# Kernel optimization log

Measured on AMD Instinct MI355X. Metric: run time of the kernel, lower is better.

Reference implementation:

```python
import jax, jax.numpy as jnp
import numpy as np

V = 50000   # vocab_size
D = 128     # embed_dim
B = 2048    # number of (center, contexts) pairs
C = 20      # context window size


def setup_inputs() -> dict:
    key = jax.random.key(0)
    ks = jax.random.split(key, 12)
    s = 0.05
    inp = {
        "center_id": jax.random.randint(ks[0], (B,), 0, V),
        "context_ids": jax.random.randint(ks[1], (B, C), 0, V),
        "epsilon": jax.random.normal(ks[2], (D,), dtype=jnp.float32),
        # parameters (torch Linear convention: W is [out, in])
        "embeddings": jax.random.normal(ks[3], (V, D), dtype=jnp.float32) * s,
        "prior_locs": jax.random.normal(ks[4], (V, D), dtype=jnp.float32) * s,
        "prior_scales": jax.random.normal(ks[5], (V, D), dtype=jnp.float32) * s,
        "W_enc": jax.random.normal(ks[6], (2 * D, 2 * D), dtype=jnp.float32) * s,
        "b_enc": jnp.zeros((2 * D,), dtype=jnp.float32),
        "W_loc": jax.random.normal(ks[7], (D, 2 * D), dtype=jnp.float32) * s,
        "b_loc": jnp.zeros((D,), dtype=jnp.float32),
        "W_scale": jax.random.normal(ks[8], (D, 2 * D), dtype=jnp.float32) * s,
        "b_scale": jnp.zeros((D,), dtype=jnp.float32),
        "W_vocab": jax.random.normal(ks[9], (V, D), dtype=jnp.float32) * s,
        "b_vocab": jnp.zeros((V,), dtype=jnp.float32),
    }
    return inp


def reference(center_id, context_ids, epsilon, embeddings, prior_locs, prior_scales,
              W_enc, b_enc, W_loc, b_loc, W_scale, b_scale, W_vocab, b_vocab):
    # Embedding lookups
    center_embed = embeddings[center_id]              # [B, D]
    context_embeds = embeddings[context_ids]          # [B, C, D]
    center_rep = jnp.broadcast_to(center_embed[:, None, :], context_embeds.shape)
    enc_in = jnp.concatenate([center_rep, context_embeds], axis=2)  # [B, C, 2D]

    # Encoder + sum over context
    h = jax.nn.relu(jnp.einsum('bcd,ed->bce', enc_in, W_enc) + b_enc)
    h = jnp.sum(h, axis=1)                            # [B, 2D]

    loc = h @ W_loc.T + b_loc                         # [B, D]
    scale = jax.nn.softplus(h @ W_scale.T + b_scale)  # [B, D]

    # Reparameterized sample (single shared epsilon, as in original)
    z = loc + scale * epsilon                         # [B, D]

    # Categorical over vocab; log-softmax == log(softmax) stably
    logits = z @ W_vocab.T + b_vocab                  # [B, V]
    log_cat = jax.nn.log_softmax(logits, axis=1)

    # Log-likelihood: sum_k log p(context_k | z)  (vectorized gather-reduce)
    lls = jnp.take_along_axis(log_cat, context_ids, axis=1).sum(axis=1)  # [B]

    # Closed-form diagonal-Gaussian KL( N(loc, scale^2) || N(ploc, pscale^2) )
    prior_loc = prior_locs[center_id]
    prior_scale = jax.nn.softplus(prior_scales[center_id])
    var0 = scale ** 2
    var1 = prior_scale ** 2
    kl = jnp.sum(jnp.log(prior_scale / scale) + (var0 + (loc - prior_loc) ** 2) / (2.0 * var1) - 0.5,
                 axis=1)                              # [B]

    elbo = lls - kl
    return jnp.mean(-elbo)
```

## Files before the change

kernel.cpp:

```cpp
#include <hip/hip_runtime.h>
#include <math.h>

#define VSZ 50000
#define VPAD 50176
#define DD  128
#define BB  2048
#define CC  20
#define E2  256

#define NCHK 98
#define CH_COLS 512
#define NRB 16
#define NWG (NCHK * NRB)

typedef short short8 __attribute__((ext_vector_type(8)));
typedef float f32x4  __attribute__((ext_vector_type(4)));

#define LOG2E 1.44269504f

__device__ __forceinline__ float softplusf(float x) {
  if (x > 20.f) return x;
  if (x < -20.f) return __expf(x);
  return log1pf(__expf(x));
}

__device__ __forceinline__ unsigned short f2bf(float f) {
  unsigned u = __float_as_uint(f);
  u = (u + 0x7fffu + ((u >> 16) & 1u)) >> 16;
  return (unsigned short)u;
}

__device__ __forceinline__ void gload_lds16(const void* g, void* l) {
  __builtin_amdgcn_global_load_lds(
      (const __attribute__((address_space(1))) unsigned int*)g,
      (__attribute__((address_space(3))) unsigned int*)l, 16, 0, 0);
}

#define NV4 1600000
#define NE4 16384
#define NL4 8192
__global__ __launch_bounds__(256) void convert_all_kernel(
    const float* __restrict__ Wv, const float* __restrict__ We,
    const float* __restrict__ Wl, const float* __restrict__ Wsc,
    ushort4* __restrict__ wv_bf, ushort4* __restrict__ we_bf,
    ushort4* __restrict__ wls_bf, float* __restrict__ S)
{
  const int gtid = blockIdx.x * 256 + threadIdx.x;
  const int stride = gridDim.x * 256;
  if (gtid < BB) S[gtid] = 0.f;
  if (gtid < (VPAD - VSZ) * 32) {
    ushort4 z; z.x = 0; z.y = 0; z.z = 0; z.w = 0;
    wv_bf[(size_t)VSZ * 32 + gtid] = z;
  }
  const int total = NV4 + NE4 + 2 * NL4;
  for (int idx = gtid; idx < total; idx += stride) {
    const float4* src; ushort4* dst; int off;
    if (idx < NV4)                   { src = (const float4*)Wv;  dst = wv_bf;  off = idx; }
    else if (idx < NV4 + NE4)        { src = (const float4*)We;  dst = we_bf;  off = idx - NV4; }
    else if (idx < NV4 + NE4 + NL4)  { src = (const float4*)Wl;  dst = wls_bf; off = idx - NV4 - NE4; }
    else { src = (const float4*)Wsc; dst = wls_bf + NL4;         off = idx - NV4 - NE4 - NL4; }
    float4 v = src[off];
    ushort4 o;
    o.x = f2bf(v.x); o.y = f2bf(v.y); o.z = f2bf(v.z); o.w = f2bf(v.w);
    dst[off] = o;
  }
}

__global__ __launch_bounds__(256) void enc_mfma_kernel(
    const int* __restrict__ center_id, const int* __restrict__ context_ids,
    const float* __restrict__ embeddings,
    const unsigned short* __restrict__ we_bf, const float* __restrict__ b_enc,
    unsigned short* __restrict__ h_bf)
{
  const int b    = blockIdx.x;
  const int tid  = threadIdx.x;
  const int wave = tid >> 6, lane = tid & 63;
  const int lr = lane & 15;
  const int lk = lane >> 4;

  __shared__ __align__(16) unsigned short ebd[21][136];

  for (int i = tid; i < 21 * 32; i += 256) {
    const int row = i >> 5, q = i & 31;
    const int src = (row < CC) ? context_ids[b * CC + row] : center_id[b];
    float4 v = ((const float4*)(embeddings + (size_t)src * DD))[q];
    ushort4 o;
    o.x = f2bf(v.x); o.y = f2bf(v.y); o.z = f2bf(v.z); o.w = f2bf(v.w);
    *(ushort4*)&ebd[row][q * 4] = o;
  }
  __syncthreads();

  f32x4 acc[2][4];
  #pragma unroll
  for (int rt = 0; rt < 2; rt++)
    #pragma unroll
    for (int ct = 0; ct < 4; ct++) acc[rt][ct] = (f32x4){0.f, 0.f, 0.f, 0.f};

  const bool r1ok = (16 + lr) < CC;

  #pragma unroll
  for (int step = 0; step < 4; step++) {
    const int k0 = step * 32 + lk * 8;
    short8 a = *(const short8*)&ebd[20][k0];
    #pragma unroll
    for (int ct = 0; ct < 4; ct++) {
      const int e = (wave * 4 + ct) * 16 + lr;
      short8 w = *(const short8*)(we_bf + (size_t)e * E2 + k0);
      acc[0][ct] = __builtin_amdgcn_mfma_f32_16x16x32_bf16(a, w, acc[0][ct], 0, 0, 0);
      acc[1][ct] = __builtin_amdgcn_mfma_f32_16x16x32_bf16(a, w, acc[1][ct], 0, 0, 0);
    }
  }
  #pragma unroll
  for (int step = 4; step < 8; step++) {
    const int k0 = step * 32 + lk * 8;
    const int kk = k0 - DD;
    short8 a0 = *(const short8*)&ebd[lr][kk];
    short8 a1 = r1ok ? *(const short8*)&ebd[16 + lr][kk] : (short8)0;
    #pragma unroll
    for (int ct = 0; ct < 4; ct++) {
      const int e = (wave * 4 + ct) * 16 + lr;
      short8 w = *(const short8*)(we_bf + (size_t)e * E2 + k0);
      acc[0][ct] = __builtin_amdgcn_mfma_f32_16x16x32_bf16(a0, w, acc[0][ct], 0, 0, 0);
      acc[1][ct] = __builtin_amdgcn_mfma_f32_16x16x32_bf16(a1, w, acc[1][ct], 0, 0, 0);
    }
  }

  float be[4], p[4];
  #pragma unroll
  for (int ct = 0; ct < 4; ct++) { be[ct] = b_enc[(wave * 4 + ct) * 16 + lr]; p[ct] = 0.f; }
  #pragma unroll
  for (int rt = 0; rt < 2; rt++) {
    #pragma unroll
    for (int j = 0; j < 4; j++) {
      const int row = rt * 16 + lk * 4 + j;
      if (row < CC) {
        #pragma unroll
        for (int ct = 0; ct < 4; ct++) p[ct] += fmaxf(acc[rt][ct][j] + be[ct], 0.f);
      }
    }
  }
  #pragma unroll
  for (int ct = 0; ct < 4; ct++) {
    p[ct] += __shfl_xor(p[ct], 16);
    p[ct] += __shfl_xor(p[ct], 32);
  }
  if (lk == 0) {
    #pragma unroll
    for (int ct = 0; ct < 4; ct++)
      h_bf[(size_t)b * E2 + (wave * 4 + ct) * 16 + lr] = f2bf(p[ct]);
  }
}

__global__ __launch_bounds__(256) void ls_post_kernel(
    const int* __restrict__ center_id, const int* __restrict__ context_ids,
    const float* __restrict__ eps,
    const float* __restrict__ prior_locs, const float* __restrict__ prior_scales,
    const unsigned short* __restrict__ h_bf, const unsigned short* __restrict__ wls_bf,
    const float* __restrict__ b_loc, const float* __restrict__ b_scale,
    const float* __restrict__ W_vocab, const float* __restrict__ b_vocab,
    unsigned short* __restrict__ zbf, float* __restrict__ base)
{
  const int b0   = blockIdx.x * 8;
  const int tid  = threadIdx.x;
  const int wave = tid >> 6, lane = tid & 63;
  const int lr = lane & 15, lk = lane >> 4;

  __shared__ __align__(16) float loc_s[8][DD];
  __shared__ __align__(16) float scale_s[8][DD];
  __shared__ __align__(16) float zsh[8][DD];
  __shared__ float klv[8], ctxacc[8];

  if (tid < 8) ctxacc[tid] = 0.f;

  f32x4 acc[4];
  #pragma unroll
  for (int ct = 0; ct < 4; ct++) acc[ct] = (f32x4){0.f, 0.f, 0.f, 0.f};

  #pragma unroll
  for (int step = 0; step < 8; step++) {
    const int k0 = step * 32 + lk * 8;
    short8 a = (lr < 8) ? *(const short8*)(h_bf + (size_t)(b0 + lr) * E2 + k0) : (short8)0;
    #pragma unroll
    for (int ct = 0; ct < 4; ct++) {
      const int o = (wave * 4 + ct) * 16 + lr;
      short8 w = *(const short8*)(wls_bf + (size_t)o * E2 + k0);
      acc[ct] = __builtin_amdgcn_mfma_f32_16x16x32_bf16(a, w, acc[ct], 0, 0, 0);
    }
  }
  #pragma unroll
  for (int ct = 0; ct < 4; ct++) {
    const int o = (wave * 4 + ct) * 16 + lr;
    #pragma unroll
    for (int j = 0; j < 4; j++) {
      const int br = lk * 4 + j;
      if (br < 8) {
        const float v = acc[ct][j];
        if (o < DD) loc_s[br][o] = v + b_loc[o];
        else        scale_s[br][o - DD] = softplusf(v + b_scale[o - DD]);
      }
    }
  }
  __syncthreads();

  if (tid < 128) {
    const int bi = tid >> 4, d0 = (tid & 15) * 8;
    const int cid = center_id[b0 + bi];
    const float* pl = prior_locs  + (size_t)cid * DD + d0;
    const float* ps = prior_scales + (size_t)cid * DD + d0;
    float kacc = 0.f;
    short8 zb;
    #pragma unroll
    for (int q = 0; q < 8; q++) {
      const float loc = loc_s[bi][d0 + q], scl = scale_s[bi][d0 + q];
      const float z = fmaf(scl, eps[d0 + q], loc);
      zsh[bi][d0 + q] = z;
      zb[q] = (short)f2bf(z * LOG2E);
      const float ploc = pl[q];
      const float pscl = softplusf(ps[q]);
      const float dd = loc - ploc;
      kacc += logf(pscl / scl) + (scl * scl + dd * dd) / (2.f * pscl * pscl) - 0.5f;
    }
    *(short8*)(zbf + (size_t)(b0 + bi) * DD + d0) = zb;
    #pragma unroll
    for (int off = 1; off < 16; off <<= 1) kacc += __shfl_xor(kacc, off, 16);
    if ((tid & 15) == 0) klv[bi] = kacc;
  }
  __syncthreads();

  for (int idx = tid; idx < 8 * CC; idx += 256) {
    const int db = idx / CC, c = idx - db * CC;
    const int vid = context_ids[(size_t)(b0 + db) * CC + c];
    const float4* wv = (const float4*)(W_vocab + (size_t)vid * DD);
    const float4* zz = (const float4*)(&zsh[db][0]);
    float dsum = b_vocab[vid];
    #pragma unroll 8
    for (int q = 0; q < DD / 4; q++) {
      float4 w = wv[q], z4 = zz[q];
      dsum = fmaf(w.x, z4.x, dsum); dsum = fmaf(w.y, z4.y, dsum);
      dsum = fmaf(w.z, z4.z, dsum); dsum = fmaf(w.w, z4.w, dsum);
    }
    atomicAdd(&ctxacc[db], dsum);
  }
  __syncthreads();

  if (tid < 8) base[b0 + tid] = klv[tid] - ctxacc[tid];
}

__global__ __launch_bounds__(256) void logits_mfma_kernel(
    const unsigned short* __restrict__ zbf, const unsigned short* __restrict__ wbf,
    const float* __restrict__ b_vocab, float* __restrict__ S)
{
  __shared__ __align__(16) char lds[2][16384];

  const int tid  = threadIdx.x;
  const int wave = tid >> 6, lane = tid & 63;
  const int lr = lane & 15;
  const int lk = lane >> 4;

  const int swz = (blockIdx.x & 7) * (NWG / 8) + (blockIdx.x >> 3);
  const int ch  = swz >> 4;
  const int rb  = swz & 15;
  const size_t cbase = (size_t)ch * (CH_COLS * 256);
  const int row0 = rb * 128 + wave * 32;

  short8 a[2][4];
  #pragma unroll
  for (int rt = 0; rt < 2; rt++)
    #pragma unroll
    for (int kk = 0; kk < 4; kk++)
      a[rt][kk] = *(const short8*)(zbf + (size_t)(row0 + rt * 16 + lr) * DD + kk * 32 + lk * 8);

#define STAGE(buf, st) do {                                                    \
    _Pragma("unroll")                                                          \
    for (int i_ = 0; i_ < 4; i_++) {                                           \
      const int c_ = (wave * 4 + i_) * 4 + (lane >> 4);                        \
      const size_t go_ = cbase + (size_t)(st) * 16384 +                        \
                         (size_t)c_ * 256 + (size_t)(((lane & 15) ^ (c_ & 15)) << 4); \
      gload_lds16((const char*)wbf + go_, &lds[(buf)][(wave * 4 + i_) * 1024]);\
    }                                                                          \
  } while (0)

  STAGE(0, 0);

  float Ssum[2][4];
  #pragma unroll
  for (int rt = 0; rt < 2; rt++)
    #pragma unroll
    for (int j = 0; j < 4; j++) Ssum[rt][j] = 0.f;

  __syncthreads();

  #pragma unroll
  for (int step = 0; step < 8; step++) {
    const int buf = step & 1;
    if (step + 1 < 8) STAGE(buf ^ 1, step + 1);

    float ebv[4];
    #pragma unroll
    for (int ct = 0; ct < 4; ct++) {
      const int g = ch * CH_COLS + step * 64 + ct * 16 + lr;
      const float bv = b_vocab[g < VSZ ? g : (VSZ - 1)];
      ebv[ct] = (g < VSZ) ? exp2f(bv * LOG2E) : 0.f;
    }

    const char* lb = &lds[buf][0];
    #pragma unroll
    for (int ct = 0; ct < 4; ct++) {
      short8 bf[4];
      #pragma unroll
      for (int kk = 0; kk < 4; kk++)
        bf[kk] = *(const short8*)(lb + (ct * 16 + lr) * 256 + (((kk * 4 + lk) ^ lr) << 4));
      f32x4 acc0 = (f32x4){0.f, 0.f, 0.f, 0.f};
      f32x4 acc1 = (f32x4){0.f, 0.f, 0.f, 0.f};
      #pragma unroll
      for (int kk = 0; kk < 4; kk++) {
        acc0 = __builtin_amdgcn_mfma_f32_16x16x32_bf16(a[0][kk], bf[kk], acc0, 0, 0, 0);
        acc1 = __builtin_amdgcn_mfma_f32_16x16x32_bf16(a[1][kk], bf[kk], acc1, 0, 0, 0);
      }
      #pragma unroll
      for (int j = 0; j < 4; j++) {
        Ssum[0][j] = fmaf(exp2f(acc0[j]), ebv[ct], Ssum[0][j]);
        Ssum[1][j] = fmaf(exp2f(acc1[j]), ebv[ct], Ssum[1][j]);
      }
    }

    __syncthreads();
  }
#undef STAGE

  #pragma unroll
  for (int rt = 0; rt < 2; rt++)
    #pragma unroll
    for (int j = 0; j < 4; j++) {
      float s = Ssum[rt][j];
      s += __shfl_xor(s, 1, 16);
      s += __shfl_xor(s, 2, 16);
      s += __shfl_xor(s, 4, 16);
      s += __shfl_xor(s, 8, 16);
      if (lr == 0) atomicAdd(&S[row0 + rt * 16 + lk * 4 + j], s);
    }
}

__global__ __launch_bounds__(256) void fin_kernel(
    const float* __restrict__ S, const float* __restrict__ base, float* __restrict__ out)
{
  const int t = threadIdx.x;
  float local = 0.f;
  for (int b = t; b < BB; b += 256)
    local += base[b] + (float)CC * logf(S[b]);
  __shared__ float red[256];
  red[t] = local;
  __syncthreads();
  for (int off = 128; off; off >>= 1) {
    if (t < off) red[t] += red[t + off];
    __syncthreads();
  }
  if (t == 0) out[0] = red[0] / (float)BB;
}

extern "C" void kernel_launch(void* const* d_in, const int* in_sizes, int n_in,
                              void* d_out, int out_size, void* d_ws, size_t ws_size,
                              hipStream_t stream) {
  const int*   center_id    = (const int*)d_in[0];
  const int*   context_ids  = (const int*)d_in[1];
  const float* eps          = (const float*)d_in[2];
  const float* embeddings   = (const float*)d_in[3];
  const float* prior_locs   = (const float*)d_in[4];
  const float* prior_scales = (const float*)d_in[5];
  const float* W_enc        = (const float*)d_in[6];
  const float* b_enc        = (const float*)d_in[7];
  const float* W_loc        = (const float*)d_in[8];
  const float* b_loc        = (const float*)d_in[9];
  const float* W_scale      = (const float*)d_in[10];
  const float* b_scale      = (const float*)d_in[11];
  const float* W_vocab      = (const float*)d_in[12];
  const float* b_vocab      = (const float*)d_in[13];
  float* out = (float*)d_out;

  char* ws = (char*)d_ws;
  unsigned short* wv_bf  = (unsigned short*)(ws);
  unsigned short* we_bf  = (unsigned short*)(ws + 12845056);
  unsigned short* wls_bf = (unsigned short*)(ws + 12845056 + 131072);
  unsigned short* h_bf   = (unsigned short*)(ws + 12845056 + 2 * 131072);
  unsigned short* zbf    = (unsigned short*)(ws + 12845056 + 2 * 131072 + 1048576);
  float*          S      = (float*)(ws + 12845056 + 2 * 131072 + 1048576 + 524288);
  float*          base   = (float*)(ws + 12845056 + 2 * 131072 + 1048576 + 524288 + 8192);

  hipLaunchKernelGGL(convert_all_kernel, dim3(1024), dim3(256), 0, stream,
                     W_vocab, W_enc, W_loc, W_scale,
                     (ushort4*)wv_bf, (ushort4*)we_bf, (ushort4*)wls_bf, S);
  hipLaunchKernelGGL(enc_mfma_kernel, dim3(BB), dim3(256), 0, stream,
                     center_id, context_ids, embeddings, we_bf, b_enc, h_bf);
  hipLaunchKernelGGL(ls_post_kernel, dim3(BB / 8), dim3(256), 0, stream,
                     center_id, context_ids, eps, prior_locs, prior_scales,
                     h_bf, wls_bf, b_loc, b_scale, W_vocab, b_vocab, zbf, base);
  hipLaunchKernelGGL(logits_mfma_kernel, dim3(NWG), dim3(256), 0, stream,
                     zbf, wv_bf, b_vocab, S);
  hipLaunchKernelGGL(fin_kernel, dim3(1), dim3(256), 0, stream, S, base, out);
}
```

Baseline: 128.6 us.

## Fuse final reduction into logits kernel, batch two pairs per encoder block

The separate final-reduction kernel is removed; the last logits workgroup, found through an atomic counter reset in the convert kernel, now does the mean reduction. The encoder kernel processes two batch rows per workgroup so each W_enc fragment load feeds twice as many MFMAs. The context-logit dot products in ls_post read the bf16 copy of W_vocab instead of fp32, which halves that gather traffic but changes numerics slightly. The changes save one launch and some memory traffic, at the cost of a grid-wide atomic and threadfence at the end of the logits kernel.

After: 208.0 us. 61.8% more time.

```diff
diff --git a/kernel.cpp b/kernel.cpp
--- a/kernel.cpp
+++ b/kernel.cpp
@@ -28,6 +28,10 @@
   unsigned u = __float_as_uint(f);
   u = (u + 0x7fffu + ((u >> 16) & 1u)) >> 16;
   return (unsigned short)u;
+}
+
+__device__ __forceinline__ float bf2f(unsigned short s) {
+  return __uint_as_float(((unsigned)s) << 16);
 }
 
 __device__ __forceinline__ void gload_lds16(const void* g, void* l) {
@@ -43,11 +47,12 @@
     const float* __restrict__ Wv, const float* __restrict__ We,
     const float* __restrict__ Wl, const float* __restrict__ Wsc,
     ushort4* __restrict__ wv_bf, ushort4* __restrict__ we_bf,
-    ushort4* __restrict__ wls_bf, float* __restrict__ S)
+    ushort4* __restrict__ wls_bf, float* __restrict__ S, int* __restrict__ ctr)
 {
   const int gtid = blockIdx.x * 256 + threadIdx.x;
   const int stride = gridDim.x * 256;
   if (gtid < BB) S[gtid] = 0.f;
+  if (gtid == 0) *ctr = 0;
   if (gtid < (VPAD - VSZ) * 32) {
     ushort4 z; z.x = 0; z.y = 0; z.z = 0; z.w = 0;
     wv_bf[(size_t)VSZ * 32 + gtid] = z;
@@ -72,82 +77,95 @@
     const unsigned short* __restrict__ we_bf, const float* __restrict__ b_enc,
     unsigned short* __restrict__ h_bf)
 {
-  const int b    = blockIdx.x;
+  const int b0   = blockIdx.x * 2;
   const int tid  = threadIdx.x;
   const int wave = tid >> 6, lane = tid & 63;
   const int lr = lane & 15;
   const int lk = lane >> 4;
 
-  __shared__ __align__(16) unsigned short ebd[21][136];
-
-  for (int i = tid; i < 21 * 32; i += 256) {
-    const int row = i >> 5, q = i & 31;
-    const int src = (row < CC) ? context_ids[b * CC + row] : center_id[b];
+  __shared__ __align__(16) unsigned short ebd[2][21][136];
+
+  for (int i = tid; i < 2 * 21 * 32; i += 256) {
+    const int bb = i / (21 * 32), r = (i >> 5) % 21, q = i & 31;
+    const int src = (r < CC) ? context_ids[(b0 + bb) * CC + r] : center_id[b0 + bb];
     float4 v = ((const float4*)(embeddings + (size_t)src * DD))[q];
     ushort4 o;
     o.x = f2bf(v.x); o.y = f2bf(v.y); o.z = f2bf(v.z); o.w = f2bf(v.w);
-    *(ushort4*)&ebd[row][q * 4] = o;
-  }
-  __syncthreads();
-
-  f32x4 acc[2][4];
-  #pragma unroll
-  for (int rt = 0; rt < 2; rt++)
-    #pragma unroll
-    for (int ct = 0; ct < 4; ct++) acc[rt][ct] = (f32x4){0.f, 0.f, 0.f, 0.f};
+    *(ushort4*)&ebd[bb][r][q * 4] = o;
+  }
+  __syncthreads();
+
+  f32x4 acc[2][2][4];
+  #pragma unroll
+  for (int bb = 0; bb < 2; bb++)
+    #pragma unroll
+    for (int rt = 0; rt < 2; rt++)
+      #pragma unroll
+      for (int ct = 0; ct < 4; ct++) acc[bb][rt][ct] = (f32x4){0.f, 0.f, 0.f, 0.f};
 
   const bool r1ok = (16 + lr) < CC;
 
   #pragma unroll
   for (int step = 0; step < 4; step++) {
     const int k0 = step * 32 + lk * 8;
-    short8 a = *(const short8*)&ebd[20][k0];
+    short8 a0 = *(const short8*)&ebd[0][20][k0];
+    short8 a1 = *(const short8*)&ebd[1][20][k0];
     #pragma unroll
     for (int ct = 0; ct < 4; ct++) {
       const int e = (wave * 4 + ct) * 16 + lr;
       short8 w = *(const short8*)(we_bf + (size_t)e * E2 + k0);
-      acc[0][ct] = __builtin_amdgcn_mfma_f32_16x16x32_bf16(a, w, acc[0][ct], 0, 0, 0);
-      acc[1][ct] = __builtin_amdgcn_mfma_f32_16x16x32_bf16(a, w, acc[1][ct], 0, 0, 0);
+      acc[0][0][ct] = __builtin_amdgcn_mfma_f32_16x16x32_bf16(a0, w, acc[0][0][ct], 0, 0, 0);
+      acc[0][1][ct] = __builtin_amdgcn_mfma_f32_16x16x32_bf16(a0, w, acc[0][1][ct], 0, 0, 0);
+      acc[1][0][ct] = __builtin_amdgcn_mfma_f32_16x16x32_bf16(a1, w, acc[1][0][ct], 0, 0, 0);
+      acc[1][1][ct] = __builtin_amdgcn_mfma_f32_16x16x32_bf16(a1, w, acc[1][1][ct], 0, 0, 0);
     }
   }
   #pragma unroll
   for (int step = 4; step < 8; step++) {
     const int k0 = step * 32 + lk * 8;
     const int kk = k0 - DD;
-    short8 a0 = *(const short8*)&ebd[lr][kk];
-    short8 a1 = r1ok ? *(const short8*)&ebd[16 + lr][kk] : (short8)0;
+    short8 a00 = *(const short8*)&ebd[0][lr][kk];
+    short8 a01 = r1ok ? *(const short8*)&ebd[0][16 + lr][kk] : (short8)0;
+    short8 a10 = *(const short8*)&ebd[1][lr][kk];
+    short8 a11 = r1ok ? *(const short8*)&ebd[1][16 + lr][kk] : (short8)0;
     #pragma unroll
     for (int ct = 0; ct < 4; ct++) {
       const int e = (wave * 4 + ct) * 16 + lr;
       short8 w = *(const short8*)(we_bf + (size_t)e * E2 + k0);
-      acc[0][ct] = __builtin_amdgcn_mfma_f32_16x16x32_bf16(a0, w, acc[0][ct], 0, 0, 0);
-      acc[1][ct] = __builtin_amdgcn_mfma_f32_16x16x32_bf16(a1, w, acc[1][ct], 0, 0, 0);
-    }
-  }
-
-  float be[4], p[4];
-  #pragma unroll
-  for (int ct = 0; ct < 4; ct++) { be[ct] = b_enc[(wave * 4 + ct) * 16 + lr]; p[ct] = 0.f; }
-  #pragma unroll
-  for (int rt = 0; rt < 2; rt++) {
-    #pragma unroll
-    for (int j = 0; j < 4; j++) {
-      const int row = rt * 16 + lk * 4 + j;
-      if (row < CC) {
-        #pragma unroll
-        for (int ct = 0; ct < 4; ct++) p[ct] += fmaxf(acc[rt][ct][j] + be[ct], 0.f);
+      acc[0][0][ct] = __builtin_amdgcn_mfma_f32_16x16x32_bf16(a00, w, acc[0][0][ct], 0, 0, 0);
+      acc[0][1][ct] = __builtin_amdgcn_mfma_f32_16x16x32_bf16(a01, w, acc[0][1][ct], 0, 0, 0);
+      acc[1][0][ct] = __builtin_amdgcn_mfma_f32_16x16x32_bf16(a10, w, acc[1][0][ct], 0, 0, 0);
+      acc[1][1][ct] = __builtin_amdgcn_mfma_f32_16x16x32_bf16(a11, w, acc[1][1][ct], 0, 0, 0);
+    }
+  }
+
+  float be[4];
+  #pragma unroll
+  for (int ct = 0; ct < 4; ct++) be[ct] = b_enc[(wave * 4 + ct) * 16 + lr];
+  #pragma unroll
+  for (int bb = 0; bb < 2; bb++) {
+    float p[4] = {0.f, 0.f, 0.f, 0.f};
+    #pragma unroll
+    for (int rt = 0; rt < 2; rt++) {
+      #pragma unroll
+      for (int j = 0; j < 4; j++) {
+        const int row = rt * 16 + lk * 4 + j;
+        if (row < CC) {
+          #pragma unroll
+          for (int ct = 0; ct < 4; ct++) p[ct] += fmaxf(acc[bb][rt][ct][j] + be[ct], 0.f);
+        }
       }
     }
-  }
-  #pragma unroll
-  for (int ct = 0; ct < 4; ct++) {
-    p[ct] += __shfl_xor(p[ct], 16);
-    p[ct] += __shfl_xor(p[ct], 32);
-  }
-  if (lk == 0) {
-    #pragma unroll
-    for (int ct = 0; ct < 4; ct++)
-      h_bf[(size_t)b * E2 + (wave * 4 + ct) * 16 + lr] = f2bf(p[ct]);
+    #pragma unroll
+    for (int ct = 0; ct < 4; ct++) {
+      p[ct] += __shfl_xor(p[ct], 16);
+      p[ct] += __shfl_xor(p[ct], 32);
+    }
+    if (lk == 0) {
+      #pragma unroll
+      for (int ct = 0; ct < 4; ct++)
+        h_bf[(size_t)(b0 + bb) * E2 + (wave * 4 + ct) * 16 + lr] = f2bf(p[ct]);
+    }
   }
 }
 
@@ -157,7 +175,7 @@
     const float* __restrict__ prior_locs, const float* __restrict__ prior_scales,
     const unsigned short* __restrict__ h_bf, const unsigned short* __restrict__ wls_bf,
     const float* __restrict__ b_loc, const float* __restrict__ b_scale,
-    const float* __restrict__ W_vocab, const float* __restrict__ b_vocab,
+    const unsigned short* __restrict__ wv_bf, const float* __restrict__ b_vocab,
     unsigned short* __restrict__ zbf, float* __restrict__ base)
 {
   const int b0   = blockIdx.x * 8;
@@ -230,14 +248,14 @@
   for (int idx = tid; idx < 8 * CC; idx += 256) {
     const int db = idx / CC, c = idx - db * CC;
     const int vid = context_ids[(size_t)(b0 + db) * CC + c];
-    const float4* wv = (const float4*)(W_vocab + (size_t)vid * DD);
-    const float4* zz = (const float4*)(&zsh[db][0]);
+    const unsigned short* wr = wv_bf + (size_t)vid * DD;
     float dsum = b_vocab[vid];
-    #pragma unroll 8
-    for (int q = 0; q < DD / 4; q++) {
-      float4 w = wv[q], z4 = zz[q];
-      dsum = fmaf(w.x, z4.x, dsum); dsum = fmaf(w.y, z4.y, dsum);
-      dsum = fmaf(w.z, z4.z, dsum); dsum = fmaf(w.w, z4.w, dsum);
+    #pragma unroll 4
+    for (int q = 0; q < 16; q++) {
+      short8 w8 = *(const short8*)(wr + q * 8);
+      #pragma unroll
+      for (int j = 0; j < 8; j++)
+        dsum = fmaf(bf2f((unsigned short)w8[j]), zsh[db][q * 8 + j], dsum);
     }
     atomicAdd(&ctxacc[db], dsum);
   }
@@ -248,9 +266,11 @@
 
 __global__ __launch_bounds__(256) void logits_mfma_kernel(
     const unsigned short* __restrict__ zbf, const unsigned short* __restrict__ wbf,
-    const float* __restrict__ b_vocab, float* __restrict__ S)
+    const float* __restrict__ b_vocab, float* __restrict__ S,
+    const float* __restrict__ base, int* __restrict__ ctr, float* __restrict__ out)
 {
   __shared__ __align__(16) char lds[2][16384];
+  __shared__ int lastsh;
 
   const int tid  = threadIdx.x;
   const int wave = tid >> 6, lane = tid & 63;
@@ -339,23 +359,24 @@
       s += __shfl_xor(s, 8, 16);
       if (lr == 0) atomicAdd(&S[row0 + rt * 16 + lk * 4 + j], s);
     }
-}
-
-__global__ __launch_bounds__(256) void fin_kernel(
-    const float* __restrict__ S, const float* __restrict__ base, float* __restrict__ out)
-{
-  const int t = threadIdx.x;
-  float local = 0.f;
-  for (int b = t; b < BB; b += 256)
-    local += base[b] + (float)CC * logf(S[b]);
-  __shared__ float red[256];
-  red[t] = local;
-  __syncthreads();
-  for (int off = 128; off; off >>= 1) {
-    if (t < off) red[t] += red[t + off];
+
+  __threadfence();
+  if (tid == 0) lastsh = (atomicAdd(ctr, 1) == NWG - 1) ? 1 : 0;
+  __syncthreads();
+  if (lastsh) {
+    __threadfence();
+    float local = 0.f;
+    for (int b = tid; b < BB; b += 256)
+      local += base[b] + (float)CC * logf(S[b]);
+    float* red = (float*)lds;
+    red[tid] = local;
     __syncthreads();
-  }
-  if (t == 0) out[0] = red[0] / (float)BB;
+    for (int off = 128; off; off >>= 1) {
+      if (tid < off) red[tid] += red[tid + off];
+      __syncthreads();
+    }
+    if (tid == 0) out[0] = red[0] / (float)BB;
+  }
 }
 
 extern "C" void kernel_launch(void* const* d_in, const int* in_sizes, int n_in,
@@ -385,16 +406,16 @@
   unsigned short* zbf    = (unsigned short*)(ws + 12845056 + 2 * 131072 + 1048576);
   float*          S      = (float*)(ws + 12845056 + 2 * 131072 + 1048576 + 524288);
   float*          base   = (float*)(ws + 12845056 + 2 * 131072 + 1048576 + 524288 + 8192);
+  int*            ctr    = (int*)(ws + 12845056 + 2 * 131072 + 1048576 + 524288 + 2 * 8192);
 
   hipLaunchKernelGGL(convert_all_kernel, dim3(1024), dim3(256), 0, stream,
                      W_vocab, W_enc, W_loc, W_scale,
-                     (ushort4*)wv_bf, (ushort4*)we_bf, (ushort4*)wls_bf, S);
-  hipLaunchKernelGGL(enc_mfma_kernel, dim3(BB), dim3(256), 0, stream,
+                     (ushort4*)wv_bf, (ushort4*)we_bf, (ushort4*)wls_bf, S, ctr);
+  hipLaunchKernelGGL(enc_mfma_kernel, dim3(BB / 2), dim3(256), 0, stream,
                      center_id, context_ids, embeddings, we_bf, b_enc, h_bf);
   hipLaunchKernelGGL(ls_post_kernel, dim3(BB / 8), dim3(256), 0, stream,
                      center_id, context_ids, eps, prior_locs, prior_scales,
-                     h_bf, wls_bf, b_loc, b_scale, W_vocab, b_vocab, zbf, base);
+                     h_bf, wls_bf, b_loc, b_scale, wv_bf, b_vocab, zbf, base);
   hipLaunchKernelGGL(logits_mfma_kernel, dim3(NWG), dim3(256), 0, stream,
-                     zbf, wv_bf, b_vocab, S);
-  hipLaunchKernelGGL(fin_kernel, dim3(1), dim3(256), 0, stream, S, base, out);
-}
+                     zbf, wv_bf, b_vocab, S, base, ctr, out);
+}
```
